# Optimization experiments

Hardware: AMD Instinct MI355X
Metric: run time of the kernel (lower is better)

Reference implementation:

```python
import jax, jax.numpy as jnp
import numpy as np

N_NODES = 100000
N_EDGES = 1200000
D_IN, D_HID, D_OUT = 64, 64, 34


def setup_inputs() -> dict:
    key = jax.random.key(0)
    k1, k2, k3, k4 = jax.random.split(key, 4)
    x = jax.random.normal(k1, (N_NODES, D_IN), dtype=jnp.float32)
    edge_index = jax.random.randint(k2, (2, N_EDGES), 0, N_NODES, dtype=jnp.int32)
    W1 = jax.random.normal(k3, (D_IN, D_HID), dtype=jnp.float32) * (1.0 / np.sqrt(D_IN))
    b1 = jnp.zeros((D_HID,), dtype=jnp.float32)
    W2 = jax.random.normal(k4, (D_HID, D_OUT), dtype=jnp.float32) * (1.0 / np.sqrt(D_HID))
    b2 = jnp.zeros((D_OUT,), dtype=jnp.float32)
    return {"x": x, "edge_index": edge_index, "W1": W1, "b1": b1, "W2": W2, "b2": b2}


def _gcn_conv(x, W, b, src, dst, norm, n_nodes):
    """PyG GCNConv: out[i] = sum_{(j->i)} norm_e * (x @ W)[j] + b."""
    xw = x @ W                                    # [N, d_out]
    msg = xw[src] * norm[:, None]                 # per-edge gather + scale
    return jax.ops.segment_sum(msg, dst, num_segments=n_nodes) + b


def reference(x, edge_index, W1, b1, W2, b2):
    n = x.shape[0]
    # add self-loops (GCNConv default add_self_loops=True)
    loops = jnp.arange(n, dtype=edge_index.dtype)
    src = jnp.concatenate([edge_index[0], loops])
    dst = jnp.concatenate([edge_index[1], loops])
    # symmetric normalization: deg^{-1/2}[src] * deg^{-1/2}[dst], deg from dst
    deg = jax.ops.segment_sum(jnp.ones_like(src, dtype=x.dtype), dst, num_segments=n)
    dinv = jnp.where(deg > 0, jax.lax.rsqrt(jnp.maximum(deg, 1e-12)), 0.0)
    norm = dinv[src] * dinv[dst]

    h = _gcn_conv(x, W1, b1, src, dst, norm, n)
    h = jax.nn.relu(h)
    h = jax.nn.softmax(h, axis=1)  # nn.Softmax() on 2D input -> dim=1
    out = _gcn_conv(h, W2, b2, src, dst, norm, n)
    return out
```

## Files before the change

kernel.cpp:

```cpp
#include <hip/hip_runtime.h>
#include <hip/hip_fp16.h>

#define D     64
#define DOUT  34
#define CAP   44
#define BSH   7
#define BW    (1 << BSH)
#define EPB   4096
#define CCAP  26
#define NPW   2
#define TB    3
#define MSLOT 24
#define GN1   16
#define GN2   8
#define HST   72
#define P2    40

typedef _Float16 f16x8 __attribute__((ext_vector_type(8)));
typedef float    f32x4 __attribute__((ext_vector_type(4)));

__global__ void k_part(const int* __restrict__ ei, int E, int nblk, int nbins,
                       int* __restrict__ binned, int* __restrict__ cnt2d) {
    __shared__ int2 ebuf[EPB];
    __shared__ int  lcnt[1024];
    int b    = blockIdx.x;
    int base = b * EPB;
    int nE   = E - base; if (nE > EPB) nE = EPB;
    for (int i = threadIdx.x; i < nE; i += 256)
        ebuf[i] = make_int2(ei[base + i], ei[E + base + i]);
    for (int i = threadIdx.x; i < nbins; i += 256) lcnt[i] = 0;
    __syncthreads();
    for (int i = threadIdx.x; i < nE; i += 256) {
        int2 e  = ebuf[i];
        int bin = e.y >> BSH;
        int pos = atomicAdd(&lcnt[bin], 1);
        if (pos < CCAP)
            binned[((size_t)bin * nblk + b) * CCAP + pos] = (e.x << BSH) | (e.y & (BW - 1));
    }
    __syncthreads();
    for (int i = threadIdx.x; i < nbins; i += 256) {
        int c = lcnt[i]; if (c > CCAP) c = CCAP;
        cnt2d[(size_t)i * nblk + b] = c;
    }
}

__global__ void k_build(const int* __restrict__ binned, const int* __restrict__ cnt2d,
                        int nblk, int* __restrict__ cnt, float* __restrict__ dinv,
                        int* __restrict__ bucket, int N) {
    __shared__ int lc2d[512];
    __shared__ int lcnt[BW];
    __shared__ __align__(16) int lbuck[BW * CAP];
    int bin = blockIdx.x;
    int d0  = bin << BSH;
    for (int i = threadIdx.x; i < nblk; i += 256) lc2d[i] = cnt2d[(size_t)bin * nblk + i];
    for (int i = threadIdx.x; i < BW; i += 256) lcnt[i] = 0;
    __syncthreads();
    int totalSlots = nblk * CCAP;
    const int* bp = binned + (size_t)bin * nblk * CCAP;
    for (int i = threadIdx.x; i < totalSlots; i += 256) {
        int blk  = i / CCAP;
        int slot = i - blk * CCAP;
        if (slot < lc2d[blk]) {
            int p   = bp[i];
            int ld  = p & (BW - 1);
            int pos = atomicAdd(&lcnt[ld], 1);
            if (pos < CAP) lbuck[ld * CAP + pos] = p >> BSH;
        }
    }
    __syncthreads();
    int nd = N - d0; if (nd > BW) nd = BW;
    for (int i = threadIdx.x; i < nd; i += 256) {
        int c = lcnt[i];
        cnt[d0 + i]  = c;
        dinv[d0 + i] = rsqrtf((float)(c + 1));
    }
    int nv = (nd * CAP) >> 2;
    int4* gb = (int4*)(bucket + (size_t)d0 * CAP);
    const int4* lb = (const int4*)lbuck;
    for (int i = threadIdx.x; i < nv; i += 256) gb[i] = lb[i];
}

__global__ void k_wconv(const float* __restrict__ W1, const float* __restrict__ W2,
                        __half* __restrict__ W1T, __half* __restrict__ W2T) {
    for (int i = threadIdx.x; i < 4096; i += 256) {
        int n = i >> 6, k = i & 63;
        W1T[i] = __float2half(W1[k * D + n]);
        W2T[i] = (n < DOUT) ? __float2half(W2[k * DOUT + n]) : __half(0.f);
    }
}

__global__ void k_gemm1m(const float* __restrict__ x, const __half* __restrict__ W1T,
                         const float* __restrict__ dinv, __half* __restrict__ xb1, int N) {
    int lane = threadIdx.x & 63;
    int wv   = threadIdx.x >> 6;
    int m    = lane & 15;
    int q    = lane >> 4;
    int rt   = blockIdx.x * 64 + wv * 16;
    int ar = rt + m; if (ar >= N) ar = N - 1;
    const float* xr = x + (size_t)ar * D + q * 8;
    float4 t0 = *(const float4*)(xr);
    float4 t1 = *(const float4*)(xr + 4);
    float4 t2 = *(const float4*)(xr + 32);
    float4 t3 = *(const float4*)(xr + 36);
    f16x8 a0, a1;
    a0[0]=(_Float16)t0.x; a0[1]=(_Float16)t0.y; a0[2]=(_Float16)t0.z; a0[3]=(_Float16)t0.w;
    a0[4]=(_Float16)t1.x; a0[5]=(_Float16)t1.y; a0[6]=(_Float16)t1.z; a0[7]=(_Float16)t1.w;
    a1[0]=(_Float16)t2.x; a1[1]=(_Float16)t2.y; a1[2]=(_Float16)t2.z; a1[3]=(_Float16)t2.w;
    a1[4]=(_Float16)t3.x; a1[5]=(_Float16)t3.y; a1[6]=(_Float16)t3.z; a1[7]=(_Float16)t3.w;
    float dr[4];
#pragma unroll
    for (int i = 0; i < 4; ++i) {
        int rr = rt + q * 4 + i;
        dr[i] = dinv[rr < N ? rr : N - 1];
    }
    const _Float16* WT = (const _Float16*)W1T;
#pragma unroll
    for (int ct = 0; ct < 4; ++ct) {
        f16x8 b0 = *(const f16x8*)(WT + (ct * 16 + m) * D + q * 8);
        f16x8 b1 = *(const f16x8*)(WT + (ct * 16 + m) * D + 32 + q * 8);
        f32x4 acc = {0.f, 0.f, 0.f, 0.f};
        acc = __builtin_amdgcn_mfma_f32_16x16x32_f16(a0, b0, acc, 0, 0, 0);
        acc = __builtin_amdgcn_mfma_f32_16x16x32_f16(a1, b1, acc, 0, 0, 0);
#pragma unroll
        for (int i = 0; i < 4; ++i) {
            int rr = rt + q * 4 + i;
            if (rr < N) xb1[(size_t)rr * D + ct * 16 + m] = __float2half(acc[i] * dr[i]);
        }
    }
}

__device__ __forceinline__ void fma8(float* a, float4 raw, float c) {
    __half2* hp = (__half2*)&raw;
#pragma unroll
    for (int k = 0; k < 4; ++k) {
        float2 f = __half22float2(hp[k]);
        a[2 * k]     = fmaf(f.x, c, a[2 * k]);
        a[2 * k + 1] = fmaf(f.y, c, a[2 * k + 1]);
    }
}

__global__ void __launch_bounds__(512, 8)
k_gather1(const int* __restrict__ cnt, const int* __restrict__ bucket,
          const __half* __restrict__ xb1, const float* __restrict__ dinv,
          const float* __restrict__ b1, const __half* __restrict__ W2T,
          __half* __restrict__ xb2, int N) {
    __shared__ int lcnt[GN1];
    __shared__ int meta[GN1 * MSLOT];
    __shared__ __align__(16) _Float16 hls[GN1 * HST];
    int tid  = threadIdx.x;
    int base = blockIdx.x * GN1;
    if (tid < GN1) lcnt[tid] = cnt[base + tid];
    {
        int4* mb = (int4*)meta;
        for (int i = tid; i < GN1 * (MSLOT / 4); i += 512) {
            int node = i / (MSLOT / 4);
            int v    = i - node * (MSLOT / 4);
            mb[i] = ((const int4*)(bucket + (size_t)(base + node) * CAP))[v];
        }
    }
    __syncthreads();
    int lane = tid & 63, w = tid >> 6;
    int g = lane >> 3, gl = lane & 7;
    int l0 = w * NPW;
    float4 buf[NPW][TB];
    float4 sr[NPW];
    int    nn[NPW];
#pragma unroll
    for (int j = 0; j < NPW; ++j) {
        int n = lcnt[l0 + j]; if (n > CAP) n = CAP;
        nn[j] = n;
        sr[j] = *((const float4*)(xb1 + (size_t)(base + l0 + j) * D) + gl);
#pragma unroll
        for (int t = 0; t < TB; ++t) {
            if (8 * t < n) {
                int idx = g + 8 * t;
                int mv = meta[(l0 + j) * MSLOT + idx];
                mv = (idx < n) ? mv : 0;
                buf[j][t] = *((const float4*)(xb1 + ((size_t)mv << 6)) + gl);
            }
        }
    }
    float acc[NPW][8];
#pragma unroll
    for (int j = 0; j < NPW; ++j) {
#pragma unroll
        for (int k = 0; k < 8; ++k) acc[j][k] = 0.f;
#pragma unroll
        for (int t = 0; t < TB; ++t) {
            if (8 * t < nn[j]) {
                float wv = (g + 8 * t < nn[j]) ? 1.f : 0.f;
                fma8(acc[j], buf[j][t], wv);
            }
        }
        for (int t = TB; 8 * t < nn[j]; ++t) {
            int idx = g + 8 * t;
            int mv = (idx < nn[j]) ? bucket[(size_t)(base + l0 + j) * CAP + idx] : 0;
            float4 bx = *((const float4*)(xb1 + ((size_t)mv << 6)) + gl);
            fma8(acc[j], bx, (idx < nn[j]) ? 1.f : 0.f);
        }
    }
    const float4* b1v = (const float4*)b1;
    float4 bb0 = b1v[2 * gl], bb1 = b1v[2 * gl + 1];
    float bArr[8] = {bb0.x, bb0.y, bb0.z, bb0.w, bb1.x, bb1.y, bb1.z, bb1.w};
#pragma unroll
    for (int j = 0; j < NPW; ++j) {
#pragma unroll
        for (int k = 0; k < 8; ++k) {
            acc[j][k] += __shfl_xor(acc[j][k], 8);
            acc[j][k] += __shfl_xor(acc[j][k], 16);
            acc[j][k] += __shfl_xor(acc[j][k], 32);
        }
        fma8(acc[j], sr[j], 1.f);
        float di = dinv[base + l0 + j];
        float m = 0.f;
#pragma unroll
        for (int k = 0; k < 8; ++k) {
            acc[j][k] = fmaxf(fmaf(acc[j][k], di, bArr[k]), 0.f);
            m = fmaxf(m, acc[j][k]);
        }
#pragma unroll
        for (int o = 4; o >= 1; o >>= 1) m = fmaxf(m, __shfl_xor(m, o));
        float s = 0.f;
#pragma unroll
        for (int k = 0; k < 8; ++k) { acc[j][k] = __expf(acc[j][k] - m); s += acc[j][k]; }
#pragma unroll
        for (int o = 4; o >= 1; o >>= 1) s += __shfl_xor(s, o);
        float inv = 1.f / s;
        if (g == 0) {
            float4 st;
            __half2* sp = (__half2*)&st;
            sp[0] = __floats2half2_rn(acc[j][0] * inv, acc[j][1] * inv);
            sp[1] = __floats2half2_rn(acc[j][2] * inv, acc[j][3] * inv);
            sp[2] = __floats2half2_rn(acc[j][4] * inv, acc[j][5] * inv);
            sp[3] = __floats2half2_rn(acc[j][6] * inv, acc[j][7] * inv);
            *((float4*)(hls + (l0 + j) * HST) + gl) = st;
        }
    }
    __syncthreads();
    if (w < 3) {
        int m16 = lane & 15, q = lane >> 4;
        f16x8 a0 = *(const f16x8*)(hls + m16 * HST + q * 8);
        f16x8 a1 = *(const f16x8*)(hls + m16 * HST + 32 + q * 8);
        const _Float16* WT = (const _Float16*)W2T;
        f16x8 wb0 = *(const f16x8*)(WT + (w * 16 + m16) * D + q * 8);
        f16x8 wb1 = *(const f16x8*)(WT + (w * 16 + m16) * D + 32 + q * 8);
        f32x4 cacc = {0.f, 0.f, 0.f, 0.f};
        cacc = __builtin_amdgcn_mfma_f32_16x16x32_f16(a0, wb0, cacc, 0, 0, 0);
        cacc = __builtin_amdgcn_mfma_f32_16x16x32_f16(a1, wb1, cacc, 0, 0, 0);
        int col = w * 16 + m16;
        if (col < P2) {
#pragma unroll
            for (int i = 0; i < 4; ++i) {
                int r = base + q * 4 + i;
                xb2[(size_t)r * P2 + col] = __float2half(cacc[i] * dinv[r]);
            }
        }
    }
}

__global__ void __launch_bounds__(256, 8)
k_gather2(const int* __restrict__ cnt, const int* __restrict__ bucket,
          const __half* __restrict__ xb2, const float* __restrict__ dinv,
          const float* __restrict__ b2, float* __restrict__ out, int N) {
    __shared__ int lcnt[GN2];
    __shared__ int meta[GN2 * MSLOT];
    int tid  = threadIdx.x;
    int base = blockIdx.x * GN2;
    if (tid < GN2) lcnt[tid] = cnt[base + tid];
    {
        int4* mb = (int4*)meta;
        for (int i = tid; i < GN2 * (MSLOT / 4); i += 256) {
            int node = i / (MSLOT / 4);
            int v    = i - node * (MSLOT / 4);
            mb[i] = ((const int4*)(bucket + (size_t)(base + node) * CAP))[v];
        }
    }
    __syncthreads();
    int lane = tid & 63, w = tid >> 6;
    int g = lane >> 3, gl = lane & 7;
    int l0 = w * NPW;
    float4 buf[NPW][TB];
    float4 sr[NPW];
    int    nn[NPW];
#pragma unroll
    for (int j = 0; j < NPW; ++j) {
        int n = lcnt[l0 + j]; if (n > CAP) n = CAP;
        nn[j] = n;
        sr[j] = make_float4(0.f, 0.f, 0.f, 0.f);
        if (gl < 5)
            sr[j] = *(const float4*)(xb2 + (size_t)(base + l0 + j) * P2 + gl * 8);
#pragma unroll
        for (int t = 0; t < TB; ++t) {
            if (8 * t < n) {
                int idx = g + 8 * t;
                int mv = meta[(l0 + j) * MSLOT + idx];
                mv = (idx < n) ? mv : 0;
                buf[j][t] = make_float4(0.f, 0.f, 0.f, 0.f);
                if (gl < 5)
                    buf[j][t] = *(const float4*)(xb2 + (size_t)mv * P2 + gl * 8);
            }
        }
    }
    float acc[NPW][8];
#pragma unroll
    for (int j = 0; j < NPW; ++j) {
#pragma unroll
        for (int k = 0; k < 8; ++k) acc[j][k] = 0.f;
#pragma unroll
        for (int t = 0; t < TB; ++t) {
            if (8 * t < nn[j]) {
                float wv = (g + 8 * t < nn[j]) ? 1.f : 0.f;
                fma8(acc[j], buf[j][t], wv);
            }
        }
        for (int t = TB; 8 * t < nn[j]; ++t) {
            int idx = g + 8 * t;
            int mv = (idx < nn[j]) ? bucket[(size_t)(base + l0 + j) * CAP + idx] : 0;
            float4 bx = make_float4(0.f, 0.f, 0.f, 0.f);
            if (gl < 5)
                bx = *(const float4*)(xb2 + (size_t)mv * P2 + gl * 8);
            fma8(acc[j], bx, (idx < nn[j]) ? 1.f : 0.f);
        }
    }
#pragma unroll
    for (int j = 0; j < NPW; ++j) {
#pragma unroll
        for (int k = 0; k < 8; ++k) {
            acc[j][k] += __shfl_xor(acc[j][k], 8);
            acc[j][k] += __shfl_xor(acc[j][k], 16);
            acc[j][k] += __shfl_xor(acc[j][k], 32);
        }
        fma8(acc[j], sr[j], 1.f);
        int r = base + l0 + j;
        float di = dinv[r];
        if (g == 0) {
            int f = 8 * gl;
#pragma unroll
            for (int k = 0; k < 8; ++k)
                if (f + k < DOUT) out[(size_t)r * DOUT + f + k] = fmaf(acc[j][k], di, b2[f + k]);
        }
    }
}

extern "C" void kernel_launch(void* const* d_in, const int* in_sizes, int n_in,
                              void* d_out, int out_size, void* d_ws, size_t ws_size,
                              hipStream_t stream) {
    const float* x  = (const float*)d_in[0];
    const int*   ei = (const int*)d_in[1];
    const float* W1 = (const float*)d_in[2];
    const float* b1 = (const float*)d_in[3];
    const float* W2 = (const float*)d_in[4];
    const float* b2 = (const float*)d_in[5];
    float* out = (float*)d_out;

    const int N = in_sizes[0] / D;
    const int E = in_sizes[1] / 2;
    const int nbins = (N + BW - 1) >> BSH;
    const int nblk  = (E + EPB - 1) / EPB;

    char*   ws     = (char*)d_ws;
    int*    cnt    = (int*)ws;
    float*  dinv   = (float*)(ws + (size_t)N * 4);
    int*    bucket = (int*)(ws + (size_t)N * 8);
    char*   U      = ws + (size_t)N * 8 + (size_t)N * CAP * 4;
    int*    binned = (int*)U;
    int*    cnt2d  = (int*)(U + (size_t)nbins * nblk * CCAP * 4);
    __half* xb1    = (__half*)U;
    __half* xb2    = xb1 + (size_t)N * D;
    __half* W1T    = (__half*)(U + (size_t)2 * N * D * 2);
    __half* W2T    = W1T + 4096;

    k_part   <<<nblk, 256, 0, stream>>>(ei, E, nblk, nbins, binned, cnt2d);
    k_build  <<<nbins, 256, 0, stream>>>(binned, cnt2d, nblk, cnt, dinv, bucket, N);
    k_wconv  <<<1, 256, 0, stream>>>(W1, W2, W1T, W2T);
    k_gemm1m <<<(N + 63) / 64, 256, 0, stream>>>(x, W1T, dinv, xb1, N);
    k_gather1<<<N / GN1, 512, 0, stream>>>(cnt, bucket, xb1, dinv, b1, W2T, xb2, N);
    k_gather2<<<N / GN2, 256, 0, stream>>>(cnt, bucket, xb2, dinv, b2, out, N);
}
```

Baseline: 226.1 us.

## Replace LDS binned CSR build with global atomic scatter and pad xb2 to 64

Replaces the two-pass shared-memory binning (k_part/k_build) with a zero kernel, a global-atomic scatter of edges into per-node buckets, and a separate dinv kernel. Also widens the layer-2 intermediate from 40 to 64 half columns so gather loads are unconditional full rows. This cuts kernel count complexity and branches but relies on contended global atomics with random destinations and reads more bytes per gathered row.

```diff
diff --git a/kernel.cpp b/kernel.cpp
--- a/kernel.cpp
+++ b/kernel.cpp
@@ -4,80 +4,38 @@
 #define D     64
 #define DOUT  34
 #define CAP   44
-#define BSH   7
-#define BW    (1 << BSH)
-#define EPB   4096
-#define CCAP  26
 #define NPW   2
 #define TB    3
 #define MSLOT 24
 #define GN1   16
 #define GN2   8
 #define HST   72
-#define P2    40
 
 typedef _Float16 f16x8 __attribute__((ext_vector_type(8)));
 typedef float    f32x4 __attribute__((ext_vector_type(4)));
 
-__global__ void k_part(const int* __restrict__ ei, int E, int nblk, int nbins,
-                       int* __restrict__ binned, int* __restrict__ cnt2d) {
-    __shared__ int2 ebuf[EPB];
-    __shared__ int  lcnt[1024];
-    int b    = blockIdx.x;
-    int base = b * EPB;
-    int nE   = E - base; if (nE > EPB) nE = EPB;
-    for (int i = threadIdx.x; i < nE; i += 256)
-        ebuf[i] = make_int2(ei[base + i], ei[E + base + i]);
-    for (int i = threadIdx.x; i < nbins; i += 256) lcnt[i] = 0;
-    __syncthreads();
-    for (int i = threadIdx.x; i < nE; i += 256) {
-        int2 e  = ebuf[i];
-        int bin = e.y >> BSH;
-        int pos = atomicAdd(&lcnt[bin], 1);
-        if (pos < CCAP)
-            binned[((size_t)bin * nblk + b) * CCAP + pos] = (e.x << BSH) | (e.y & (BW - 1));
-    }
-    __syncthreads();
-    for (int i = threadIdx.x; i < nbins; i += 256) {
-        int c = lcnt[i]; if (c > CCAP) c = CCAP;
-        cnt2d[(size_t)i * nblk + b] = c;
-    }
-}
-
-__global__ void k_build(const int* __restrict__ binned, const int* __restrict__ cnt2d,
-                        int nblk, int* __restrict__ cnt, float* __restrict__ dinv,
-                        int* __restrict__ bucket, int N) {
-    __shared__ int lc2d[512];
-    __shared__ int lcnt[BW];
-    __shared__ __align__(16) int lbuck[BW * CAP];
-    int bin = blockIdx.x;
-    int d0  = bin << BSH;
-    for (int i = threadIdx.x; i < nblk; i += 256) lc2d[i] = cnt2d[(size_t)bin * nblk + i];
-    for (int i = threadIdx.x; i < BW; i += 256) lcnt[i] = 0;
-    __syncthreads();
-    int totalSlots = nblk * CCAP;
-    const int* bp = binned + (size_t)bin * nblk * CCAP;
-    for (int i = threadIdx.x; i < totalSlots; i += 256) {
-        int blk  = i / CCAP;
-        int slot = i - blk * CCAP;
-        if (slot < lc2d[blk]) {
-            int p   = bp[i];
-            int ld  = p & (BW - 1);
-            int pos = atomicAdd(&lcnt[ld], 1);
-            if (pos < CAP) lbuck[ld * CAP + pos] = p >> BSH;
-        }
-    }
-    __syncthreads();
-    int nd = N - d0; if (nd > BW) nd = BW;
-    for (int i = threadIdx.x; i < nd; i += 256) {
-        int c = lcnt[i];
-        cnt[d0 + i]  = c;
-        dinv[d0 + i] = rsqrtf((float)(c + 1));
-    }
-    int nv = (nd * CAP) >> 2;
-    int4* gb = (int4*)(bucket + (size_t)d0 * CAP);
-    const int4* lb = (const int4*)lbuck;
-    for (int i = threadIdx.x; i < nv; i += 256) gb[i] = lb[i];
+__global__ void k_zero(int* __restrict__ cnt, int N) {
+    int i = blockIdx.x * 256 + threadIdx.x;
+    int stride = gridDim.x * 256;
+    for (; i < N; i += stride) cnt[i] = 0;
+}
+
+__global__ void k_scatter(const int* __restrict__ ei, int E,
+                          int* __restrict__ cnt, int* __restrict__ bucket) {
+    int i = blockIdx.x * 256 + threadIdx.x;
+    int stride = gridDim.x * 256;
+    for (; i < E; i += stride) {
+        int s = ei[i];
+        int d = ei[E + i];
+        int pos = atomicAdd(&cnt[d], 1);
+        if (pos < CAP) bucket[(size_t)d * CAP + pos] = s;
+    }
+}
+
+__global__ void k_dinv(const int* __restrict__ cnt, float* __restrict__ dinv, int N) {
+    int i = blockIdx.x * 256 + threadIdx.x;
+    int stride = gridDim.x * 256;
+    for (; i < N; i += stride) dinv[i] = rsqrtf((float)(cnt[i] + 1));
 }
 
 __global__ void k_wconv(const float* __restrict__ W1, const float* __restrict__ W2,
@@ -237,7 +195,7 @@
         }
     }
     __syncthreads();
-    if (w < 3) {
+    if (w < 4) {
         int m16 = lane & 15, q = lane >> 4;
         f16x8 a0 = *(const f16x8*)(hls + m16 * HST + q * 8);
         f16x8 a1 = *(const f16x8*)(hls + m16 * HST + 32 + q * 8);
@@ -247,13 +205,10 @@
         f32x4 cacc = {0.f, 0.f, 0.f, 0.f};
         cacc = __builtin_amdgcn_mfma_f32_16x16x32_f16(a0, wb0, cacc, 0, 0, 0);
         cacc = __builtin_amdgcn_mfma_f32_16x16x32_f16(a1, wb1, cacc, 0, 0, 0);
-        int col = w * 16 + m16;
-        if (col < P2) {
-#pragma unroll
-            for (int i = 0; i < 4; ++i) {
-                int r = base + q * 4 + i;
-                xb2[(size_t)r * P2 + col] = __float2half(cacc[i] * dinv[r]);
-            }
+#pragma unroll
+        for (int i = 0; i < 4; ++i) {
+            int r = base + q * 4 + i;
+            xb2[(size_t)r * D + w * 16 + m16] = __float2half(cacc[i] * dinv[r]);
         }
     }
 }
@@ -286,18 +241,14 @@
     for (int j = 0; j < NPW; ++j) {
         int n = lcnt[l0 + j]; if (n > CAP) n = CAP;
         nn[j] = n;
-        sr[j] = make_float4(0.f, 0.f, 0.f, 0.f);
-        if (gl < 5)
-            sr[j] = *(const float4*)(xb2 + (size_t)(base + l0 + j) * P2 + gl * 8);
+        sr[j] = *((const float4*)(xb2 + (size_t)(base + l0 + j) * D) + gl);
 #pragma unroll
         for (int t = 0; t < TB; ++t) {
             if (8 * t < n) {
                 int idx = g + 8 * t;
                 int mv = meta[(l0 + j) * MSLOT + idx];
                 mv = (idx < n) ? mv : 0;
-                buf[j][t] = make_float4(0.f, 0.f, 0.f, 0.f);
-                if (gl < 5)
-                    buf[j][t] = *(const float4*)(xb2 + (size_t)mv * P2 + gl * 8);
+                buf[j][t] = *((const float4*)(xb2 + ((size_t)mv << 6)) + gl);
             }
         }
     }
@@ -316,9 +267,7 @@
         for (int t = TB; 8 * t < nn[j]; ++t) {
             int idx = g + 8 * t;
             int mv = (idx < nn[j]) ? bucket[(size_t)(base + l0 + j) * CAP + idx] : 0;
-            float4 bx = make_float4(0.f, 0.f, 0.f, 0.f);
-            if (gl < 5)
-                bx = *(const float4*)(xb2 + (size_t)mv * P2 + gl * 8);
+            float4 bx = *((const float4*)(xb2 + ((size_t)mv << 6)) + gl);
             fma8(acc[j], bx, (idx < nn[j]) ? 1.f : 0.f);
         }
     }
@@ -355,23 +304,19 @@
 
     const int N = in_sizes[0] / D;
     const int E = in_sizes[1] / 2;
-    const int nbins = (N + BW - 1) >> BSH;
-    const int nblk  = (E + EPB - 1) / EPB;
 
     char*   ws     = (char*)d_ws;
     int*    cnt    = (int*)ws;
     float*  dinv   = (float*)(ws + (size_t)N * 4);
     int*    bucket = (int*)(ws + (size_t)N * 8);
-    char*   U      = ws + (size_t)N * 8 + (size_t)N * CAP * 4;
-    int*    binned = (int*)U;
-    int*    cnt2d  = (int*)(U + (size_t)nbins * nblk * CCAP * 4);
-    __half* xb1    = (__half*)U;
+    __half* xb1    = (__half*)(ws + (size_t)N * 8 + (size_t)N * CAP * 4);
     __half* xb2    = xb1 + (size_t)N * D;
-    __half* W1T    = (__half*)(U + (size_t)2 * N * D * 2);
+    __half* W1T    = xb2 + (size_t)N * D;
     __half* W2T    = W1T + 4096;
 
-    k_part   <<<nblk, 256, 0, stream>>>(ei, E, nblk, nbins, binned, cnt2d);
-    k_build  <<<nbins, 256, 0, stream>>>(binned, cnt2d, nblk, cnt, dinv, bucket, N);
+    k_zero   <<<128, 256, 0, stream>>>(cnt, N);
+    k_scatter<<<1024, 256, 0, stream>>>(ei, E, cnt, bucket);
+    k_dinv   <<<128, 256, 0, stream>>>(cnt, dinv, N);
     k_wconv  <<<1, 256, 0, stream>>>(W1, W2, W1T, W2T);
     k_gemm1m <<<(N + 63) / 64, 256, 0, stream>>>(x, W1T, dinv, xb1, N);
     k_gather1<<<N / GN1, 512, 0, stream>>>(cnt, bucket, xb1, dinv, b1, W2T, xb2, N);
```

Result: slower. 281.8 us (+24.6%).
